# Performance work log

Hardware: AMD Instinct MI355X
Metric: run time of the kernel (lower is better)

Reference implementation:

```python
import jax, jax.numpy as jnp
import numpy as np

B = 64            # decode batch (one new token per sequence)
H = 32            # query heads
HKV = 2           # kv heads (multi_query_group_num)
D = 128           # head_size (kv_channels)
HID = 4096        # hidden size
ROT = D // 2      # ChatGLM applies rotary to first half of head dims
BLOCK = 16        # paged-cache block size
NBLK = 16384      # total blocks
MAX_S = 4096
ROPE_BASE = 10000.0


def setup_inputs() -> dict:
    key = jax.random.key(0)
    ks = jax.random.split(key, 8)
    hidden_states = jax.random.normal(ks[0], (B, HID), jnp.float32)
    wqkv = jax.random.normal(ks[1], (H * D + 2 * HKV * D, HID), jnp.float32) * 0.02
    wdense = jax.random.normal(ks[2], (HID, H * D), jnp.float32) * 0.02
    k_cache = jax.random.normal(ks[3], (NBLK, BLOCK, HKV, D), jnp.float32)
    v_cache = jax.random.normal(ks[4], (NBLK, BLOCK, HKV, D), jnp.float32)
    # disjoint block tables: sequence b owns blocks [b*256, (b+1)*256)
    block_tables = jnp.arange(B * (MAX_S // BLOCK), dtype=jnp.int32).reshape(B, MAX_S // BLOCK)
    input_lengths = jax.random.randint(ks[5], (B,), 1024, MAX_S + 1, dtype=jnp.int32)
    # slot of the current token = position input_lengths-1 within its block table
    pos = input_lengths - 1
    slots = block_tables[jnp.arange(B), pos // BLOCK] * BLOCK + pos % BLOCK
    return {"hidden_states": hidden_states, "wqkv": wqkv, "wdense": wdense,
            "k_cache": k_cache, "v_cache": v_cache, "block_tables": block_tables,
            "slots": slots, "input_lengths": input_lengths, "max_s": MAX_S}


def _apply_rope(x, positions):
    # x: [B, h, D]; GPT-J interleaved rope on first ROT dims (ChatGLM style)
    inv_freq = 1.0 / (ROPE_BASE ** (jnp.arange(0, ROT, 2, dtype=jnp.float32) / ROT))  # [ROT/2]
    ang = positions.astype(jnp.float32)[:, None] * inv_freq[None, :]                  # [B, ROT/2]
    c = jnp.cos(ang)[:, None, :]  # [B,1,ROT/2]
    s = jnp.sin(ang)[:, None, :]
    xr = x[..., :ROT].reshape(*x.shape[:-1], ROT // 2, 2)
    x0, x1 = xr[..., 0], xr[..., 1]
    rot = jnp.stack([x0 * c - x1 * s, x1 * c + x0 * s], axis=-1).reshape(*x.shape[:-1], ROT)
    return jnp.concatenate([rot, x[..., ROT:]], axis=-1)


def reference(hidden_states, wqkv, wdense, k_cache, v_cache, block_tables, slots, input_lengths, max_s):
    G = H // HKV
    scale = D ** -0.5
    positions = input_lengths - 1

    qkv = hidden_states @ wqkv.T                                   # [B, 4608]
    q, k, v = jnp.split(qkv, [H * D, H * D + HKV * D], axis=1)
    q = q.reshape(B, H, D)
    k = k.reshape(B, HKV, D)
    v = v.reshape(B, HKV, D)

    q = _apply_rope(q, positions)
    k = _apply_rope(k, positions)

    # reshape_and_cache: scatter current token's K/V into the paged cache
    kc = k_cache.reshape(NBLK * BLOCK, HKV, D).at[slots].set(k)
    vc = v_cache.reshape(NBLK * BLOCK, HKV, D).at[slots].set(v)

    # paged attention: gather per-sequence KV via block tables
    s_idx = jnp.arange(max_s)
    flat = block_tables[:, s_idx // BLOCK] * BLOCK + s_idx % BLOCK  # [B, S]
    K = kc[flat]                                                    # [B, S, HKV, D]
    V = vc[flat]

    q4 = q.reshape(B, HKV, G, D).astype(jnp.float32)
    scores = jnp.einsum('bkgd,bskd->bkgs', q4, K.astype(jnp.float32)) * scale  # [B,HKV,G,S]
    mask = s_idx[None, :] < input_lengths[:, None]                  # [B, S]
    scores = jnp.where(mask[:, None, None, :], scores, -jnp.inf)
    probs = jax.nn.softmax(scores, axis=-1)
    out = jnp.einsum('bkgs,bskd->bkgd', probs, V.astype(jnp.float32))  # [B,HKV,G,D]
    out = out.reshape(B, H * D).astype(hidden_states.dtype)
    return out @ wdense.T
```

## Files before the change

### kernel.cpp

```cpp
#include <hip/hip_runtime.h>
#include <math.h>

#define KDIM 4096
#define SPLITS 8
#define WAYS 32
#define MAXPB 256
#define NQKV 4608
#define NDENSE 4096
#define KSPLIT 16
#define KRANGE 256

typedef __attribute__((ext_vector_type(8))) short bh8;
typedef __attribute__((ext_vector_type(4))) float f32x4;

__device__ __forceinline__ short f2bf(float x) {
    union { float f; unsigned u; } v; v.f = x;
    unsigned r = v.u + 0x7FFFu + ((v.u >> 16) & 1u);
    return (short)(r >> 16);
}
__device__ __forceinline__ float bf2f(short h) {
    union { unsigned u; float f; } v;
    v.u = ((unsigned)(unsigned short)h) << 16;
    return v.f;
}

__device__ __forceinline__ void rope_rotate(float& x0, float& x1, int j, int pos) {
    double inv = pow(10000.0, -(double)j / 32.0);
    double ang = (double)pos * inv;
    float c = (float)cos(ang), s = (float)sin(ang);
    float r0 = x0 * c - x1 * s;
    float r1 = x1 * c + x0 * s;
    x0 = r0; x1 = r1;
}

__global__ __launch_bounds__(256) void prep_hilo_pk(
    const float* __restrict__ x, unsigned short* __restrict__ hi,
    unsigned short* __restrict__ lo)
{
    const int id = blockIdx.x * 256 + threadIdx.x;
    const int lane = id & 63;
    const int mtkt = id >> 6;
    const int mt = mtkt & 3;
    const int kt = mtkt >> 2;
    const int m = mt * 16 + (lane & 15);
    const int kk = kt * 32 + (lane >> 4) * 8;
    const float* src = &x[(size_t)m * KDIM + kk];
    float4 a = *(const float4*)src;
    float4 b = *(const float4*)(src + 4);
    float vf[8] = {a.x, a.y, a.z, a.w, b.x, b.y, b.z, b.w};
    unsigned short hbuf[8], lbuf[8];
    #pragma unroll
    for (int e = 0; e < 8; ++e) {
        short hh = f2bf(vf[e]);
        hbuf[e] = (unsigned short)hh;
        lbuf[e] = (unsigned short)f2bf(vf[e] - bf2f(hh));
    }
    *(int4*)&hi[(size_t)id * 8] = *(int4*)hbuf;
    *(int4*)&lo[(size_t)id * 8] = *(int4*)lbuf;
}

__global__ __launch_bounds__(256) void gemm_mfma(
    const unsigned short* __restrict__ A_hi, const unsigned short* __restrict__ A_lo,
    const float* __restrict__ W, float* __restrict__ part, int N)
{
    const int tid = threadIdx.x;
    const int wv = tid >> 6;
    const int l = tid & 63;
    const int lr = l & 15;
    const int h = l >> 4;
    const int n0 = blockIdx.x * 64 + wv * 16;
    const int ks = blockIdx.y;
    const int k0 = ks * KRANGE;

    const float* wrow = &W[(size_t)(n0 + lr) * KDIM + h * 8];
    const size_t abase = (size_t)ks * 8 * 4 * 512 + (size_t)l * 8;

    f32x4 acc[4];
    #pragma unroll
    for (int mt = 0; mt < 4; ++mt) acc[mt] = (f32x4){0.f, 0.f, 0.f, 0.f};

    float4 w00, w01, w10, w11;
    bh8 ahc[4], alc[4], ahn[4], aln[4];

    w00 = *(const float4*)&wrow[k0];
    w01 = *(const float4*)&wrow[k0 + 4];
    w10 = *(const float4*)&wrow[k0 + 32];
    w11 = *(const float4*)&wrow[k0 + 36];
    #pragma unroll
    for (int mt = 0; mt < 4; ++mt) {
        ahc[mt] = *(const bh8*)&A_hi[abase + (size_t)mt * 512];
        alc[mt] = *(const bh8*)&A_lo[abase + (size_t)mt * 512];
    }

    auto body = [&](float4& pwa, float4& pwb, int kt) {
        float4 cw0 = pwa, cw1 = pwb;
        if (kt + 2 < 8) {
            pwa = *(const float4*)&wrow[k0 + (kt + 2) * 32];
            pwb = *(const float4*)&wrow[k0 + (kt + 2) * 32 + 4];
        }
        if (kt + 1 < 8) {
            const size_t an = abase + (size_t)(kt + 1) * 2048;
            #pragma unroll
            for (int mt = 0; mt < 4; ++mt) {
                ahn[mt] = *(const bh8*)&A_hi[an + (size_t)mt * 512];
                aln[mt] = *(const bh8*)&A_lo[an + (size_t)mt * 512];
            }
        }
        bh8 whi, wlo;
        float wf[8] = {cw0.x, cw0.y, cw0.z, cw0.w, cw1.x, cw1.y, cw1.z, cw1.w};
        #pragma unroll
        for (int e = 0; e < 8; ++e) {
            short hh = f2bf(wf[e]);
            whi[e] = hh;
            wlo[e] = f2bf(wf[e] - bf2f(hh));
        }
        #pragma unroll
        for (int mt = 0; mt < 4; ++mt) {
            acc[mt] = __builtin_amdgcn_mfma_f32_16x16x32_bf16(ahc[mt], whi, acc[mt], 0, 0, 0);
            acc[mt] = __builtin_amdgcn_mfma_f32_16x16x32_bf16(alc[mt], whi, acc[mt], 0, 0, 0);
            acc[mt] = __builtin_amdgcn_mfma_f32_16x16x32_bf16(ahc[mt], wlo, acc[mt], 0, 0, 0);
        }
        if (kt + 1 < 8) {
            #pragma unroll
            for (int mt = 0; mt < 4; ++mt) { ahc[mt] = ahn[mt]; alc[mt] = aln[mt]; }
        }
    };

    for (int kt2 = 0; kt2 < 4; ++kt2) {
        body(w00, w01, kt2 * 2);
        body(w10, w11, kt2 * 2 + 1);
    }

    #pragma unroll
    for (int mt = 0; mt < 4; ++mt) {
        const int m = mt * 16 + h * 4;
        #pragma unroll
        for (int j = 0; j < 4; ++j)
            part[((size_t)ks * 64 + m + j) * N + n0 + lr] = acc[mt][j];
    }
}

__global__ __launch_bounds__(256) void reduce_qkv(
    const float* __restrict__ part, const int* __restrict__ lens,
    float* __restrict__ q_rope, float* __restrict__ knew, float* __restrict__ vnew)
{
    const int b = blockIdx.y;
    const int c0 = (blockIdx.x * 256 + threadIdx.x) * 2;
    float x0 = 0.f, x1 = 0.f;
    #pragma unroll
    for (int ks = 0; ks < KSPLIT; ++ks) {
        float2 v = *(const float2*)&part[((size_t)ks * 64 + b) * NQKV + c0];
        x0 += v.x; x1 += v.y;
    }
    const int pos = lens[b] - 1;
    if (c0 < 4096) {
        const int d = c0 & 127;
        if (d < 64) rope_rotate(x0, x1, d >> 1, pos);
        q_rope[(size_t)b * 4096 + c0] = x0;
        q_rope[(size_t)b * 4096 + c0 + 1] = x1;
    } else if (c0 < 4352) {
        const int kidx = c0 - 4096, kh = kidx >> 7, d = kidx & 127;
        if (d < 64) rope_rotate(x0, x1, d >> 1, pos);
        knew[(b * 2 + kh) * 128 + d] = x0;
        knew[(b * 2 + kh) * 128 + d + 1] = x1;
    } else {
        const int vidx = c0 - 4352, kh = vidx >> 7, d = vidx & 127;
        vnew[(b * 2 + kh) * 128 + d] = x0;
        vnew[(b * 2 + kh) * 128 + d + 1] = x1;
    }
}

__global__ __launch_bounds__(256) void attn_mfma(
    const float* __restrict__ qr, const float* __restrict__ knew,
    const float* __restrict__ vnew, const float* __restrict__ kcache,
    const float* __restrict__ vcache, const int* __restrict__ bt,
    const int* __restrict__ lens, float* __restrict__ pO, float* __restrict__ pML)
{
    const int split = blockIdx.x;
    const int kh = blockIdx.y;
    const int b = blockIdx.z;
    const int tid = threadIdx.x;
    const int wv = tid >> 6;
    const int l = tid & 63;
    const int g = l & 15;
    const int h = l >> 4;
    const int way = split * 4 + wv;

    __shared__ unsigned int sP[4][256];
    __shared__ float sO[3][16][132];
    __shared__ float sML[3][2][16];

    const int len = lens[b];
    const int nchunks = (len + 31) >> 5;
    const size_t nbase = ((size_t)(b * 2 + kh)) * 128;

    const float scale = 0.08838834764831845f;
    bh8 qf[4];
    {
        const float* qrow = &qr[((size_t)(b * 32 + kh * 16 + g)) * 128 + h * 8];
        #pragma unroll
        for (int dc = 0; dc < 4; ++dc) {
            float4 a = *(const float4*)&qrow[dc * 32];
            float4 c = *(const float4*)&qrow[dc * 32 + 4];
            qf[dc][0] = f2bf(a.x * scale); qf[dc][1] = f2bf(a.y * scale);
            qf[dc][2] = f2bf(a.z * scale); qf[dc][3] = f2bf(a.w * scale);
            qf[dc][4] = f2bf(c.x * scale); qf[dc][5] = f2bf(c.y * scale);
            qf[dc][6] = f2bf(c.z * scale); qf[dc][7] = f2bf(c.w * scale);
        }
    }

    float m = -INFINITY, lacc = 0.f;
    f32x4 oacc[8];
    #pragma unroll
    for (int dt = 0; dt < 8; ++dt) oacc[dt] = (f32x4){0.f, 0.f, 0.f, 0.f};

    for (int c = way; c < nchunks; c += WAYS) {
        const int s0 = c * 32;
        const int blk0 = bt[b * MAXPB + 2 * c];
        const int blk1 = bt[b * MAXPB + 2 * c + 1];

        const float* rowK0 = (s0 + g == len - 1) ? &knew[nbase]
            : &kcache[(((size_t)blk0 * 16 + g) * 2 + kh) * 128];
        const float* rowK1 = (s0 + 16 + g == len - 1) ? &knew[nbase]
            : &kcache[(((size_t)blk1 * 16 + g) * 2 + kh) * 128];
        float4 k0[8], k1[8];
        #pragma unroll
        for (int dc = 0; dc < 4; ++dc) {
            k0[2*dc]   = *(const float4*)&rowK0[dc * 32 + h * 8];
            k0[2*dc+1] = *(const float4*)&rowK0[dc * 32 + h * 8 + 4];
            k1[2*dc]   = *(const float4*)&rowK1[dc * 32 + h * 8];
            k1[2*dc+1] = *(const float4*)&rowK1[dc * 32 + h * 8 + 4];
        }

        float vv[8][8];
        #pragma unroll
        for (int e = 0; e < 8; ++e) {
            const int p = h * 8 + e;
            const int s = s0 + p;
            const float* rowV = (s == len - 1) ? &vnew[nbase]
                : &vcache[(((size_t)(p < 16 ? blk0 : blk1) * 16 + (p & 15)) * 2 + kh) * 128];
            #pragma unroll
            for (int dt = 0; dt < 8; ++dt)
                vv[e][dt] = rowV[dt * 16 + g];
        }

        f32x4 sa0 = (f32x4){0.f,0.f,0.f,0.f};
        f32x4 sa1 = (f32x4){0.f,0.f,0.f,0.f};
        #pragma unroll
        for (int dc = 0; dc < 4; ++dc) {
            bh8 a0, a1;
            a0[0]=f2bf(k0[2*dc].x);   a0[1]=f2bf(k0[2*dc].y);
            a0[2]=f2bf(k0[2*dc].z);   a0[3]=f2bf(k0[2*dc].w);
            a0[4]=f2bf(k0[2*dc+1].x); a0[5]=f2bf(k0[2*dc+1].y);
            a0[6]=f2bf(k0[2*dc+1].z); a0[7]=f2bf(k0[2*dc+1].w);
            a1[0]=f2bf(k1[2*dc].x);   a1[1]=f2bf(k1[2*dc].y);
            a1[2]=f2bf(k1[2*dc].z);   a1[3]=f2bf(k1[2*dc].w);
            a1[4]=f2bf(k1[2*dc+1].x); a1[5]=f2bf(k1[2*dc+1].y);
            a1[6]=f2bf(k1[2*dc+1].z); a1[7]=f2bf(k1[2*dc+1].w);
            sa0 = __builtin_amdgcn_mfma_f32_16x16x32_bf16(a0, qf[dc], sa0, 0, 0, 0);
            sa1 = __builtin_amdgcn_mfma_f32_16x16x32_bf16(a1, qf[dc], sa1, 0, 0, 0);
        }

        float sc[8];
        #pragma unroll
        for (int j = 0; j < 4; ++j) {
            sc[j]     = (s0 + 4*h + j      < len) ? sa0[j] : -INFINITY;
            sc[4 + j] = (s0 + 16 + 4*h + j < len) ? sa1[j] : -INFINITY;
        }
        float tmax = sc[0];
        #pragma unroll
        for (int j = 1; j < 8; ++j) tmax = fmaxf(tmax, sc[j]);
        tmax = fmaxf(tmax, __shfl_xor(tmax, 16));
        tmax = fmaxf(tmax, __shfl_xor(tmax, 32));
        const float m_new = fmaxf(m, tmax);
        const float corr = expf(m - m_new);
        float pe[8], ls = 0.f;
        #pragma unroll
        for (int j = 0; j < 8; ++j) { pe[j] = expf(sc[j] - m_new); ls += pe[j]; }
        ls += __shfl_xor(ls, 16);
        ls += __shfl_xor(ls, 32);
        lacc = lacc * corr + ls;
        m = m_new;
        #pragma unroll
        for (int dt = 0; dt < 8; ++dt) {
            oacc[dt][0] *= corr; oacc[dt][1] *= corr;
            oacc[dt][2] *= corr; oacc[dt][3] *= corr;
        }

        unsigned int* myP = sP[wv];
        #pragma unroll
        for (int ph = 0; ph < 2; ++ph)
            #pragma unroll
            for (int t2 = 0; t2 < 2; ++t2) {
                unsigned lo = (unsigned short)f2bf(pe[ph*4 + 2*t2]);
                unsigned hi = (unsigned short)f2bf(pe[ph*4 + 2*t2 + 1]);
                myP[g * 16 + ph * 8 + 2 * h + t2] = lo | (hi << 16);
            }
        asm volatile("s_waitcnt lgkmcnt(0)" ::: "memory");
        bh8 pf = *(const bh8*)&myP[g * 16 + 4 * h];

        #pragma unroll
        for (int dt = 0; dt < 8; ++dt) {
            bh8 av;
            #pragma unroll
            for (int e = 0; e < 8; ++e) av[e] = f2bf(vv[e][dt]);
            oacc[dt] = __builtin_amdgcn_mfma_f32_16x16x32_bf16(av, pf, oacc[dt], 0, 0, 0);
        }
    }

    if (wv > 0) {
        #pragma unroll
        for (int dt = 0; dt < 8; ++dt)
            #pragma unroll
            for (int j = 0; j < 4; ++j)
                sO[wv-1][g][dt*16 + 4*h + j] = oacc[dt][j];
        if (l < 16) {
            sML[wv-1][0][g] = m;
            sML[wv-1][1][g] = lacc;
        }
    }
    __syncthreads();
    if (wv == 0) {
        float M = m;
        #pragma unroll
        for (int i = 0; i < 3; ++i) M = fmaxf(M, sML[i][0][g]);
        const float w0 = expf(m - M);
        float L = lacc * w0;
        float wi[3];
        #pragma unroll
        for (int i = 0; i < 3; ++i) {
            wi[i] = expf(sML[i][0][g] - M);
            L += sML[i][1][g] * wi[i];
        }
        size_t base = ((((size_t)(b * 2 + kh)) * SPLITS + split) * 16 + g) * 128;
        #pragma unroll
        for (int dt = 0; dt < 8; ++dt)
            #pragma unroll
            for (int j = 0; j < 4; ++j) {
                float o = oacc[dt][j] * w0;
                #pragma unroll
                for (int i = 0; i < 3; ++i)
                    o += sO[i][g][dt*16 + 4*h + j] * wi[i];
                pO[base + dt*16 + 4*h + j] = o;
            }
        if (l < 16) {
            size_t mb = ((((size_t)(b * 2 + kh)) * SPLITS + split) * 16 + g) * 2;
            pML[mb] = M;
            pML[mb + 1] = L;
        }
    }
}

__global__ __launch_bounds__(256) void attn_combine(
    const float* __restrict__ pO, const float* __restrict__ pML,
    unsigned short* __restrict__ a_hi, unsigned short* __restrict__ a_lo)
{
    const int bk = blockIdx.x;
    const int tid = threadIdx.x;
    const int g = tid >> 4;
    const int dh = tid & 15;

    float ms[SPLITS], ls[SPLITS];
    float M = -INFINITY;
    #pragma unroll
    for (int s = 0; s < SPLITS; ++s) {
        size_t mb = (((size_t)bk * SPLITS + s) * 16 + g) * 2;
        ms[s] = pML[mb]; ls[s] = pML[mb + 1];
        M = fmaxf(M, ms[s]);
    }
    float L = 0.f;
    #pragma unroll
    for (int s = 0; s < SPLITS; ++s) L += ls[s] * expf(ms[s] - M);

    float acc[8] = {0, 0, 0, 0, 0, 0, 0, 0};
    #pragma unroll
    for (int s = 0; s < SPLITS; ++s) {
        float wgt = expf(ms[s] - M);
        const float* src = &pO[(((size_t)bk * SPLITS + s) * 16 + g) * 128 + dh * 8];
        #pragma unroll
        for (int r = 0; r < 8; ++r) acc[r] += wgt * src[r];
    }
    const float invL = 1.f / L;
    const int b = bk >> 1, kh = bk & 1;
    const int k0 = (kh * 16 + g) * 128 + dh * 8;
    const int kt = k0 >> 5;
    const int h2 = dh & 3;
    const size_t didx = (((size_t)(kt * 4 + (b >> 4))) * 64 + h2 * 16 + (b & 15)) * 8;
    unsigned short hbuf[8], lbuf[8];
    #pragma unroll
    for (int r = 0; r < 8; ++r) {
        float o = acc[r] * invL;
        short hh = f2bf(o);
        hbuf[r] = (unsigned short)hh;
        lbuf[r] = (unsigned short)f2bf(o - bf2f(hh));
    }
    *(int4*)&a_hi[didx] = *(int4*)hbuf;
    *(int4*)&a_lo[didx] = *(int4*)lbuf;
}

__global__ __launch_bounds__(256) void reduce_dense(
    const float* __restrict__ part, float* __restrict__ out)
{
    const int b = blockIdx.y;
    const int col = (blockIdx.x * 256 + threadIdx.x) * 4;
    float4 s = make_float4(0.f, 0.f, 0.f, 0.f);
    #pragma unroll
    for (int ks = 0; ks < KSPLIT; ++ks) {
        float4 v = *(const float4*)&part[((size_t)ks * 64 + b) * NDENSE + col];
        s.x += v.x; s.y += v.y; s.z += v.z; s.w += v.w;
    }
    *(float4*)&out[(size_t)b * 4096 + col] = s;
}

extern "C" void kernel_launch(void* const* d_in, const int* in_sizes, int n_in,
                              void* d_out, int out_size, void* d_ws, size_t ws_size,
                              hipStream_t stream) {
    const float* hidden = (const float*)d_in[0];
    const float* wqkv   = (const float*)d_in[1];
    const float* wdense = (const float*)d_in[2];
    const float* kcache = (const float*)d_in[3];
    const float* vcache = (const float*)d_in[4];
    const int*   bt     = (const int*)d_in[5];
    const int*   lens   = (const int*)d_in[7];
    float* out = (float*)d_out;

    float* ws     = (float*)d_ws;
    float* q_rope = ws;
    float* k_new  = ws + 262144;
    float* v_new  = ws + 278528;
    unsigned short* A_hi = (unsigned short*)(ws + 294912);
    unsigned short* A_lo = A_hi + 262144;
    float* regX   = ws + 557056;
    float* pO     = regX;
    float* pML    = ws + 5275648;

    prep_hilo_pk<<<dim3(128), dim3(256), 0, stream>>>(hidden, A_hi, A_lo);
    gemm_mfma<<<dim3(NQKV / 64, KSPLIT), dim3(256), 0, stream>>>(
        A_hi, A_lo, wqkv, regX, NQKV);
    reduce_qkv<<<dim3(9, 64), dim3(256), 0, stream>>>(
        regX, lens, q_rope, k_new, v_new);
    attn_mfma<<<dim3(SPLITS, 2, 64), dim3(256), 0, stream>>>(
        q_rope, k_new, v_new, kcache, vcache, bt, lens, pO, pML);
    attn_combine<<<dim3(128), dim3(256), 0, stream>>>(pO, pML, A_hi, A_lo);
    gemm_mfma<<<dim3(NDENSE / 64, KSPLIT), dim3(256), 0, stream>>>(
        A_hi, A_lo, wdense, regX, NDENSE);
    reduce_dense<<<dim3(4, 64), dim3(256), 0, stream>>>(regX, out);
}
```

Baseline: 169.7 us.

## Drop in-block wave merge in attention, write per-wave partials, widen combine

The attention kernel no longer merges its four waves through shared memory with a block barrier. Each wave now writes its own partial output and max/sum to global memory (32 ways instead of 8 splits), and the combine kernel reduces over all 32 partials with a 2D grid of 128-thread blocks. V values are converted to packed bf16 as they load, which cuts register use, and launch bounds request 5 blocks per CU for higher occupancy. The cost is four times more partial-output traffic to global memory and more work in the combine step, and the workspace offset for pML moves to fit the larger buffer.

```diff
diff --git a/kernel.cpp b/kernel.cpp
--- a/kernel.cpp
+++ b/kernel.cpp
@@ -170,7 +170,7 @@
     }
 }
 
-__global__ __launch_bounds__(256) void attn_mfma(
+__global__ __launch_bounds__(256, 5) void attn_mfma(
     const float* __restrict__ qr, const float* __restrict__ knew,
     const float* __restrict__ vnew, const float* __restrict__ kcache,
     const float* __restrict__ vcache, const int* __restrict__ bt,
@@ -187,8 +187,6 @@
     const int way = split * 4 + wv;
 
     __shared__ unsigned int sP[4][256];
-    __shared__ float sO[3][16][132];
-    __shared__ float sML[3][2][16];
 
     const int len = lens[b];
     const int nchunks = (len + 31) >> 5;
@@ -232,7 +230,7 @@
             k1[2*dc+1] = *(const float4*)&rowK1[dc * 32 + h * 8 + 4];
         }
 
-        float vv[8][8];
+        unsigned vw[8][4];
         #pragma unroll
         for (int e = 0; e < 8; ++e) {
             const int p = h * 8 + e;
@@ -240,8 +238,11 @@
             const float* rowV = (s == len - 1) ? &vnew[nbase]
                 : &vcache[(((size_t)(p < 16 ? blk0 : blk1) * 16 + (p & 15)) * 2 + kh) * 128];
             #pragma unroll
-            for (int dt = 0; dt < 8; ++dt)
-                vv[e][dt] = rowV[dt * 16 + g];
+            for (int dt = 0; dt < 8; ++dt) {
+                unsigned short bb = (unsigned short)f2bf(rowV[dt * 16 + g]);
+                if (e & 1) vw[dt][e >> 1] |= ((unsigned)bb << 16);
+                else       vw[dt][e >> 1] = bb;
+            }
         }
 
         f32x4 sa0 = (f32x4){0.f,0.f,0.f,0.f};
@@ -301,84 +302,51 @@
 
         #pragma unroll
         for (int dt = 0; dt < 8; ++dt) {
-            bh8 av;
-            #pragma unroll
-            for (int e = 0; e < 8; ++e) av[e] = f2bf(vv[e][dt]);
-            oacc[dt] = __builtin_amdgcn_mfma_f32_16x16x32_bf16(av, pf, oacc[dt], 0, 0, 0);
-        }
-    }
-
-    if (wv > 0) {
-        #pragma unroll
-        for (int dt = 0; dt < 8; ++dt)
-            #pragma unroll
-            for (int j = 0; j < 4; ++j)
-                sO[wv-1][g][dt*16 + 4*h + j] = oacc[dt][j];
-        if (l < 16) {
-            sML[wv-1][0][g] = m;
-            sML[wv-1][1][g] = lacc;
-        }
-    }
-    __syncthreads();
-    if (wv == 0) {
-        float M = m;
-        #pragma unroll
-        for (int i = 0; i < 3; ++i) M = fmaxf(M, sML[i][0][g]);
-        const float w0 = expf(m - M);
-        float L = lacc * w0;
-        float wi[3];
-        #pragma unroll
-        for (int i = 0; i < 3; ++i) {
-            wi[i] = expf(sML[i][0][g] - M);
-            L += sML[i][1][g] * wi[i];
-        }
-        size_t base = ((((size_t)(b * 2 + kh)) * SPLITS + split) * 16 + g) * 128;
-        #pragma unroll
-        for (int dt = 0; dt < 8; ++dt)
-            #pragma unroll
-            for (int j = 0; j < 4; ++j) {
-                float o = oacc[dt][j] * w0;
-                #pragma unroll
-                for (int i = 0; i < 3; ++i)
-                    o += sO[i][g][dt*16 + 4*h + j] * wi[i];
-                pO[base + dt*16 + 4*h + j] = o;
-            }
-        if (l < 16) {
-            size_t mb = ((((size_t)(b * 2 + kh)) * SPLITS + split) * 16 + g) * 2;
-            pML[mb] = M;
-            pML[mb + 1] = L;
-        }
-    }
-}
-
-__global__ __launch_bounds__(256) void attn_combine(
+            union { unsigned u[4]; bh8 v; } cvt;
+            cvt.u[0] = vw[dt][0]; cvt.u[1] = vw[dt][1];
+            cvt.u[2] = vw[dt][2]; cvt.u[3] = vw[dt][3];
+            oacc[dt] = __builtin_amdgcn_mfma_f32_16x16x32_bf16(cvt.v, pf, oacc[dt], 0, 0, 0);
+        }
+    }
+
+    size_t base = ((((size_t)(b * 2 + kh)) * 32 + way) * 16 + g) * 128;
+    #pragma unroll
+    for (int dt = 0; dt < 8; ++dt)
+        #pragma unroll
+        for (int j = 0; j < 4; ++j)
+            pO[base + dt*16 + 4*h + j] = oacc[dt][j];
+    if (l < 16) {
+        size_t mb = ((((size_t)(b * 2 + kh)) * 32 + way) * 16 + g) * 2;
+        pML[mb] = m;
+        pML[mb + 1] = lacc;
+    }
+}
+
+__global__ __launch_bounds__(128) void attn_combine(
     const float* __restrict__ pO, const float* __restrict__ pML,
     unsigned short* __restrict__ a_hi, unsigned short* __restrict__ a_lo)
 {
     const int bk = blockIdx.x;
+    const int half = blockIdx.y;
     const int tid = threadIdx.x;
-    const int g = tid >> 4;
-    const int dh = tid & 15;
-
-    float ms[SPLITS], ls[SPLITS];
+    const int g = tid >> 3;
+    const int dh = half * 8 + (tid & 7);
+
     float M = -INFINITY;
     #pragma unroll
-    for (int s = 0; s < SPLITS; ++s) {
-        size_t mb = (((size_t)bk * SPLITS + s) * 16 + g) * 2;
-        ms[s] = pML[mb]; ls[s] = pML[mb + 1];
-        M = fmaxf(M, ms[s]);
-    }
+    for (int s = 0; s < 32; ++s)
+        M = fmaxf(M, pML[(((size_t)bk * 32 + s) * 16 + g) * 2]);
+
     float L = 0.f;
-    #pragma unroll
-    for (int s = 0; s < SPLITS; ++s) L += ls[s] * expf(ms[s] - M);
-
     float acc[8] = {0, 0, 0, 0, 0, 0, 0, 0};
-    #pragma unroll
-    for (int s = 0; s < SPLITS; ++s) {
-        float wgt = expf(ms[s] - M);
-        const float* src = &pO[(((size_t)bk * SPLITS + s) * 16 + g) * 128 + dh * 8];
-        #pragma unroll
-        for (int r = 0; r < 8; ++r) acc[r] += wgt * src[r];
+    #pragma unroll 4
+    for (int s = 0; s < 32; ++s) {
+        size_t mb = (((size_t)bk * 32 + s) * 16 + g) * 2;
+        float w = expf(pML[mb] - M);
+        L += pML[mb + 1] * w;
+        const float* src = &pO[(((size_t)bk * 32 + s) * 16 + g) * 128 + dh * 8];
+        #pragma unroll
+        for (int r = 0; r < 8; ++r) acc[r] += w * src[r];
     }
     const float invL = 1.f / L;
     const int b = bk >> 1, kh = bk & 1;
@@ -432,7 +400,7 @@
     unsigned short* A_lo = A_hi + 262144;
     float* regX   = ws + 557056;
     float* pO     = regX;
-    float* pML    = ws + 5275648;
+    float* pML    = ws + 557056 + 8388608;
 
     prep_hilo_pk<<<dim3(128), dim3(256), 0, stream>>>(hidden, A_hi, A_lo);
     gemm_mfma<<<dim3(NQKV / 64, KSPLIT), dim3(256), 0, stream>>>(
@@ -441,7 +409,7 @@
         regX, lens, q_rope, k_new, v_new);
     attn_mfma<<<dim3(SPLITS, 2, 64), dim3(256), 0, stream>>>(
         q_rope, k_new, v_new, kcache, vcache, bt, lens, pO, pML);
-    attn_combine<<<dim3(128), dim3(256), 0, stream>>>(pO, pML, A_hi, A_lo);
+    attn_combine<<<dim3(128, 2), dim3(128), 0, stream>>>(pO, pML, A_hi, A_lo);
     gemm_mfma<<<dim3(NDENSE / 64, KSPLIT), dim3(256), 0, stream>>>(
         A_hi, A_lo, wdense, regX, NDENSE);
     reduce_dense<<<dim3(4, 64), dim3(256), 0, stream>>>(regX, out);
```

After: 288.2 us. 1.7x slower.
